# Optimization experiments

Measured on AMD Instinct MI355X. Metric: run time of the kernel, lower is better.

## Reference

```python
import jax, jax.numpy as jnp
import numpy as np

B, NV, NF, AOD, SD = 16384, 32, 64, 64, 512  # batch, num_variable, num_factor, adj_output_dim, state_dim
H = AOD * AOD // 2  # 2048, hyper_w1 hidden/out


def setup_inputs() -> dict:
    key = jax.random.key(0)
    ks = jax.random.split(key, 16)
    s = 0.02
    p = lambda k, shp: (s * jax.random.normal(k, shp, dtype=jnp.float32))
    return {
        "agent_emb": jax.random.normal(ks[0], (B, NV, AOD), dtype=jnp.float32),
        "states": jax.random.normal(ks[1], (B, SD), dtype=jnp.float32),
        # hyper_w1: Linear(SD,H) -> ReLU -> Linear(H,H)
        "w1a_W": p(ks[2], (SD, H)), "w1a_b": jnp.zeros((H,), jnp.float32),
        "w1b_W": p(ks[3], (H, H)), "w1b_b": jnp.zeros((H,), jnp.float32),
        # hyper_b1: Linear(SD, NV*AOD//2)
        "b1_W": p(ks[4], (SD, NV * AOD // 2)), "b1_b": jnp.zeros((NV * AOD // 2,), jnp.float32),
        # hyper_w2: Linear(SD, AOD//2*NF*2) -> ReLU -> Linear(.., AOD//2*NF)
        "w2a_W": p(ks[5], (SD, AOD // 2 * NF * 2)), "w2a_b": jnp.zeros((AOD // 2 * NF * 2,), jnp.float32),
        "w2b_W": p(ks[6], (AOD // 2 * NF * 2, AOD // 2 * NF)), "w2b_b": jnp.zeros((AOD // 2 * NF,), jnp.float32),
        # hyper_b2: Linear(SD, NV*AOD//2) -> ReLU -> Linear(.., NV*NF)
        "b2a_W": p(ks[7], (SD, NV * AOD // 2)), "b2a_b": jnp.zeros((NV * AOD // 2,), jnp.float32),
        "b2b_W": p(ks[8], (NV * AOD // 2, NV * NF)), "b2b_b": jnp.zeros((NV * NF,), jnp.float32),
    }


def reference(agent_emb, states, w1a_W, w1a_b, w1b_W, w1b_b, b1_W, b1_b,
              w2a_W, w2a_b, w2b_W, w2b_b, b2a_W, b2a_b, b2b_W, b2b_b):
    # hypernets
    w1 = (jax.nn.relu(states @ w1a_W + w1a_b) @ w1b_W + w1b_b).reshape(B, AOD, AOD // 2)
    b1 = (states @ b1_W + b1_b).reshape(B, NV, AOD // 2)
    w2 = (jax.nn.relu(states @ w2a_W + w2a_b) @ w2b_W + w2b_b).reshape(B, AOD // 2, NF)
    b2 = (jax.nn.relu(states @ b2a_W + b2a_b) @ b2b_W + b2b_b).reshape(B, NV, NF)
    # mixing: small batched matmuls + ELU
    hidden = jax.nn.elu(jnp.einsum('bva,bah->bvh', agent_emb, w1) + b1)  # [B,NV,AOD//2]
    out = jnp.einsum('bvh,bhf->bvf', hidden, w2) + b2                    # [B,NV,NF]
    # detached abs-max normalization over the variable dim, then sigmoid
    max_out = jax.lax.stop_gradient(jnp.max(jnp.abs(out), axis=1, keepdims=True)) + 1e-5
    norm = jnp.minimum(jnp.ones_like(max_out), 5.0 / max_out)
    return jax.nn.sigmoid(out * norm)
```

## Files before the change

### kernel.cpp

```cpp
#include <hip/hip_runtime.h>
#include <hip/hip_bf16.h>

#define B_    16384
#define NV_   32
#define NF_   64
#define AOD_  64
#define SD_   512
#define H_    2048
#define MC_   4096
#define NCHUNK_ 4

typedef __attribute__((ext_vector_type(8))) short short8_t;
typedef __attribute__((ext_vector_type(8))) unsigned short ushort8_t;
typedef __attribute__((ext_vector_type(4))) unsigned short ushort4_t;
typedef __attribute__((ext_vector_type(4))) float f32x4;

__device__ __forceinline__ float bf2f(unsigned short u) {
  union { unsigned int i; float f; } c; c.i = ((unsigned int)u) << 16; return c.f;
}
__device__ __forceinline__ unsigned short f2bf(float f) {
  union { float f; unsigned int i; } c; c.f = f;
  unsigned int x = c.i;
  return (unsigned short)((x + 0x7FFFu + ((x >> 16) & 1u)) >> 16);
}

__device__ __forceinline__ void gload16(const unsigned short* g, unsigned short* l) {
  __builtin_amdgcn_global_load_lds(
      (const __attribute__((address_space(1))) unsigned int*)g,
      (__attribute__((address_space(3))) unsigned int*)l, 16, 0, 0);
}


__global__ __launch_bounds__(256) void transpose_split(
    const float* __restrict__ src, unsigned short* __restrict__ dhi,
    unsigned short* __restrict__ dlo, int K, int N) {
  __shared__ float tile[32][33];
  const int nb = blockIdx.x * 32, kb = blockIdx.y * 32;
  const int tx = threadIdx.x & 31, ty = threadIdx.x >> 5;
#pragma unroll
  for (int r = 0; r < 32; r += 8)
    tile[ty + r][tx] = src[(size_t)(kb + ty + r) * N + nb + tx];
  __syncthreads();
#pragma unroll
  for (int r = 0; r < 32; r += 8) {
    const float x = tile[tx][ty + r];
    const unsigned short h = f2bf(x);
    const size_t o = (size_t)(nb + ty + r) * K + kb + tx;
    dhi[o] = h;
    dlo[o] = f2bf(x - bf2f(h));
  }
}

__global__ __launch_bounds__(256) void transpose_single(
    const float* __restrict__ src, unsigned short* __restrict__ dst, int K, int N) {
  __shared__ float tile[32][33];
  const int nb = blockIdx.x * 32, kb = blockIdx.y * 32;
  const int tx = threadIdx.x & 31, ty = threadIdx.x >> 5;
#pragma unroll
  for (int r = 0; r < 32; r += 8)
    tile[ty + r][tx] = src[(size_t)(kb + ty + r) * N + nb + tx];
  __syncthreads();
#pragma unroll
  for (int r = 0; r < 32; r += 8)
    dst[(size_t)(nb + ty + r) * K + kb + tx] = f2bf(tile[tx][ty + r]);
}

__global__ __launch_bounds__(256) void cvt_split(
    const float* __restrict__ in, unsigned short* __restrict__ hi,
    unsigned short* __restrict__ lo) {
  const int i = (blockIdx.x * 256 + threadIdx.x) * 4;
  const float4 v = *(const float4*)(in + i);
  ushort4_t oh, ol;
  oh.x = f2bf(v.x); ol.x = f2bf(v.x - bf2f(oh.x));
  oh.y = f2bf(v.y); ol.y = f2bf(v.y - bf2f(oh.y));
  oh.z = f2bf(v.z); ol.z = f2bf(v.z - bf2f(oh.z));
  oh.w = f2bf(v.w); ol.w = f2bf(v.w - bf2f(oh.w));
  *(ushort4_t*)(hi + i) = oh;
  *(ushort4_t*)(lo + i) = ol;
}

template <int ASPLIT, int BSPLIT, int OMODE>
__global__ __launch_bounds__(256) void gemm_k(
    const unsigned short* __restrict__ Ah, const unsigned short* __restrict__ Al, int lda,
    const unsigned short* __restrict__ Bh, const unsigned short* __restrict__ Bl,
    const float* __restrict__ bias,
    void* __restrict__ outH, void* __restrict__ outL, int N, int K) {
  __shared__ unsigned short lAh[128 * 32];
  __shared__ unsigned short lBh[128 * 32];
  __shared__ unsigned short lAl[ASPLIT ? 128 * 32 : 64];
  __shared__ unsigned short lBl[BSPLIT ? 128 * 32 : 64];

  const int t = threadIdx.x;
  const int w = t >> 6, l = t & 63;
  const int wm = w >> 1, wn = w & 1;
  const int lhi = l >> 4, llo = l & 15;
  const int k8 = lhi * 8;
  const int m0 = blockIdx.y * 128, n0 = blockIdx.x * 128;

  const int r1 = t >> 2, kc = (t & 3) * 8;
  const size_t aoff1 = (size_t)(m0 + r1) * lda + kc;
  const size_t aoff2 = (size_t)(m0 + r1 + 64) * lda + kc;
  const size_t boff1 = (size_t)(n0 + r1) * (size_t)K + kc;
  const size_t boff2 = (size_t)(n0 + r1 + 64) * (size_t)K + kc;
  unsigned short* const d1 = (unsigned short*)0 + w * 512;
  const int wo1 = w * 512, wo2 = 2048 + w * 512;
  (void)d1;

  f32x4 acc[4][4];
#pragma unroll
  for (int i = 0; i < 4; ++i)
#pragma unroll
    for (int j = 0; j < 4; ++j) acc[i][j] = (f32x4){0.f, 0.f, 0.f, 0.f};

  for (int kt = 0; kt < K; kt += 32) {
    gload16(Ah + aoff1 + kt, lAh + wo1);
    gload16(Ah + aoff2 + kt, lAh + wo2);
    if constexpr (ASPLIT) {
      gload16(Al + aoff1 + kt, lAl + wo1);
      gload16(Al + aoff2 + kt, lAl + wo2);
    }
    gload16(Bh + boff1 + kt, lBh + wo1);
    gload16(Bh + boff2 + kt, lBh + wo2);
    if constexpr (BSPLIT) {
      gload16(Bl + boff1 + kt, lBl + wo1);
      gload16(Bl + boff2 + kt, lBl + wo2);
    }
    __syncthreads();

    short8_t ah[4], bh[4];
#pragma unroll
    for (int i = 0; i < 4; ++i)
      ah[i] = *(const short8_t*)&lAh[(wm * 64 + i * 16 + llo) * 32 + k8];
#pragma unroll
    for (int j = 0; j < 4; ++j)
      bh[j] = *(const short8_t*)&lBh[(wn * 64 + j * 16 + llo) * 32 + k8];

    if constexpr (ASPLIT && BSPLIT) {
      short8_t al[4], bl[4];
#pragma unroll
      for (int i = 0; i < 4; ++i)
        al[i] = *(const short8_t*)&lAl[(wm * 64 + i * 16 + llo) * 32 + k8];
#pragma unroll
      for (int j = 0; j < 4; ++j)
        bl[j] = *(const short8_t*)&lBl[(wn * 64 + j * 16 + llo) * 32 + k8];
#pragma unroll
      for (int i = 0; i < 4; ++i)
#pragma unroll
        for (int j = 0; j < 4; ++j) {
          acc[i][j] = __builtin_amdgcn_mfma_f32_16x16x32_bf16(ah[i], bh[j], acc[i][j], 0, 0, 0);
          acc[i][j] = __builtin_amdgcn_mfma_f32_16x16x32_bf16(ah[i], bl[j], acc[i][j], 0, 0, 0);
          acc[i][j] = __builtin_amdgcn_mfma_f32_16x16x32_bf16(al[i], bh[j], acc[i][j], 0, 0, 0);
        }
    } else {
#pragma unroll
      for (int i = 0; i < 4; ++i)
#pragma unroll
        for (int j = 0; j < 4; ++j)
          acc[i][j] = __builtin_amdgcn_mfma_f32_16x16x32_bf16(ah[i], bh[j], acc[i][j], 0, 0, 0);
    }
    __syncthreads();
  }

#pragma unroll
  for (int j = 0; j < 4; ++j) {
    const int col = n0 + wn * 64 + j * 16 + llo;
    const float bv = bias[col];
#pragma unroll
    for (int i = 0; i < 4; ++i) {
      const int row = m0 + wm * 64 + i * 16 + lhi * 4;
#pragma unroll
      for (int r = 0; r < 4; ++r) {
        float v = acc[i][j][r] + bv;
        if constexpr (OMODE == 1 || OMODE == 2) v = fmaxf(v, 0.f);
        const size_t o = (size_t)(row + r) * N + col;
        if constexpr (OMODE == 3) {
          ((float*)outH)[o] = v;
        } else if constexpr (OMODE == 2) {
          const unsigned short h = f2bf(v);
          ((unsigned short*)outH)[o] = h;
          ((unsigned short*)outL)[o] = f2bf(v - bf2f(h));
        } else {
          ((unsigned short*)outH)[o] = f2bf(v);
        }
      }
    }
  }
}

__global__ __launch_bounds__(256) void mixing_kernel(
    const float* __restrict__ emb,
    const float* __restrict__ w1buf,
    const unsigned short* __restrict__ b1buf,
    const float* __restrict__ w2buf,
    const unsigned short* __restrict__ b2buf,
    float* __restrict__ out) {
  __shared__ float s_emb[2048];
  __shared__ float s_w1[2048];
  __shared__ float s_b1[1024];
  __shared__ float s_w2[2048];
  __shared__ float s_b2[2048];
  __shared__ float s_hid[1024];
  __shared__ float s_out[2048];
  __shared__ float s_norm[64];

  const int b = blockIdx.x, t = threadIdx.x;

  {
    const float4* src = (const float4*)(emb + (size_t)b * 2048);
    ((float4*)s_emb)[t] = src[t];
    ((float4*)s_emb)[t + 256] = src[t + 256];
  }
  {
    const float4* src = (const float4*)(w1buf + (size_t)b * 2048);
    ((float4*)s_w1)[t] = src[t];
    ((float4*)s_w1)[t + 256] = src[t + 256];
  }
  {
    const float4* src = (const float4*)(w2buf + (size_t)b * 2048);
    ((float4*)s_w2)[t] = src[t];
    ((float4*)s_w2)[t + 256] = src[t + 256];
  }
  if (t < 128) {
    ushort8_t u = *(const ushort8_t*)(b1buf + (size_t)b * 1024 + t * 8);
#pragma unroll
    for (int e = 0; e < 8; ++e) s_b1[t * 8 + e] = bf2f(u[e]);
  }
  {
    ushort8_t u = *(const ushort8_t*)(b2buf + (size_t)b * 2048 + t * 8);
#pragma unroll
    for (int e = 0; e < 8; ++e) s_b2[t * 8 + e] = bf2f(u[e]);
  }
  __syncthreads();

#pragma unroll
  for (int p = 0; p < 4; ++p) {
    const int idx = t + p * 256;
    const int v = idx >> 5, h = idx & 31;
    float acc = s_b1[idx];
#pragma unroll 8
    for (int a = 0; a < 64; ++a) acc += s_emb[v * 64 + a] * s_w1[a * 32 + h];
    s_hid[idx] = acc > 0.f ? acc : expm1f(acc);
  }
  __syncthreads();

#pragma unroll
  for (int p = 0; p < 8; ++p) {
    const int idx = t + p * 256;
    const int v = idx >> 6, f = idx & 63;
    float acc = s_b2[idx];
#pragma unroll 8
    for (int h = 0; h < 32; ++h) acc += s_hid[v * 32 + h] * s_w2[h * 64 + f];
    s_out[idx] = acc;
  }
  __syncthreads();

  if (t < 64) {
    float m = 0.f;
#pragma unroll
    for (int v = 0; v < 32; ++v) m = fmaxf(m, fabsf(s_out[v * 64 + t]));
    m += 1e-5f;
    s_norm[t] = fminf(1.0f, 5.0f / m);
  }
  __syncthreads();

#pragma unroll
  for (int p = 0; p < 8; ++p) {
    const int idx = t + p * 256;
    const float x = s_out[idx] * s_norm[idx & 63];
    out[(size_t)b * 2048 + idx] = 1.f / (1.f + expf(-x));
  }
}


extern "C" void kernel_launch(void* const* d_in, const int* in_sizes, int n_in,
                              void* d_out, int out_size, void* d_ws, size_t ws_size,
                              hipStream_t stream) {
  const float* agent_emb = (const float*)d_in[0];
  const float* states    = (const float*)d_in[1];
  const float* w1a_W = (const float*)d_in[2];  const float* w1a_b = (const float*)d_in[3];
  const float* w1b_W = (const float*)d_in[4];  const float* w1b_b = (const float*)d_in[5];
  const float* b1_W  = (const float*)d_in[6];  const float* b1_b  = (const float*)d_in[7];
  const float* w2a_W = (const float*)d_in[8];  const float* w2a_b = (const float*)d_in[9];
  const float* w2b_W = (const float*)d_in[10]; const float* w2b_b = (const float*)d_in[11];
  const float* b2a_W = (const float*)d_in[12]; const float* b2a_b = (const float*)d_in[13];
  const float* b2b_W = (const float*)d_in[14]; const float* b2b_b = (const float*)d_in[15];
  float* out = (float*)d_out;

  char* ws = (char*)d_ws;
  size_t off = 0;
  auto alloc = [&](size_t bytes) -> char* {
    char* p = ws + off;
    off = (off + bytes + 255) & ~(size_t)255;
    return p;
  };
  typedef unsigned short us;
  us* sth = (us*)alloc((size_t)B_ * SD_ * 2);
  us* stl = (us*)alloc((size_t)B_ * SD_ * 2);
  us* w1aTh = (us*)alloc((size_t)2048 * 512 * 2); us* w1aTl = (us*)alloc((size_t)2048 * 512 * 2);
  us* b1Th  = (us*)alloc((size_t)1024 * 512 * 2); us* b1Tl  = (us*)alloc((size_t)1024 * 512 * 2);
  us* w2aTh = (us*)alloc((size_t)4096 * 512 * 2); us* w2aTl = (us*)alloc((size_t)4096 * 512 * 2);
  us* b2aTh = (us*)alloc((size_t)1024 * 512 * 2); us* b2aTl = (us*)alloc((size_t)1024 * 512 * 2);
  us* w1bTh = (us*)alloc((size_t)2048 * 2048 * 2); us* w1bTl = (us*)alloc((size_t)2048 * 2048 * 2);
  us* w2bTh = (us*)alloc((size_t)2048 * 4096 * 2); us* w2bTl = (us*)alloc((size_t)2048 * 4096 * 2);
  us* b2bT  = (us*)alloc((size_t)2048 * 1024 * 2);
  us* t1h = (us*)alloc((size_t)MC_ * 2048 * 2); us* t1l = (us*)alloc((size_t)MC_ * 2048 * 2);
  us* t2h = (us*)alloc((size_t)MC_ * 4096 * 2); us* t2l = (us*)alloc((size_t)MC_ * 4096 * 2);
  us* b1buf = (us*)alloc((size_t)MC_ * 1024 * 2);
  us* t3buf = (us*)alloc((size_t)MC_ * 1024 * 2);
  float* w1buf = (float*)alloc((size_t)MC_ * 2048 * 4);
  float* w2buf = (float*)alloc((size_t)MC_ * 2048 * 4);
  us* b2buf = (us*)alloc((size_t)MC_ * 2048 * 2);
  if (off > ws_size) return;

  cvt_split<<<(B_ * SD_) / (4 * 256), 256, 0, stream>>>(states, sth, stl);
  transpose_split<<<dim3(2048 / 32, 512 / 32), 256, 0, stream>>>(w1a_W, w1aTh, w1aTl, 512, 2048);
  transpose_split<<<dim3(1024 / 32, 512 / 32), 256, 0, stream>>>(b1_W,  b1Th,  b1Tl,  512, 1024);
  transpose_split<<<dim3(4096 / 32, 512 / 32), 256, 0, stream>>>(w2a_W, w2aTh, w2aTl, 512, 4096);
  transpose_split<<<dim3(1024 / 32, 512 / 32), 256, 0, stream>>>(b2a_W, b2aTh, b2aTl, 512, 1024);
  transpose_split<<<dim3(2048 / 32, 2048 / 32), 256, 0, stream>>>(w1b_W, w1bTh, w1bTl, 2048, 2048);
  transpose_split<<<dim3(2048 / 32, 4096 / 32), 256, 0, stream>>>(w2b_W, w2bTh, w2bTl, 4096, 2048);
  transpose_single<<<dim3(2048 / 32, 1024 / 32), 256, 0, stream>>>(b2b_W, b2bT, 1024, 2048);

  for (int c = 0; c < NCHUNK_; ++c) {
    const size_t R = (size_t)c * MC_;
    const us* Ah = sth + R * SD_;
    const us* Al = stl + R * SD_;
    gemm_k<1, 1, 2><<<dim3(16, MC_ / 128), 256, 0, stream>>>(
        Ah, Al, SD_, w1aTh, w1aTl, w1a_b, t1h, t1l, 2048, SD_);
    gemm_k<1, 1, 0><<<dim3(8, MC_ / 128), 256, 0, stream>>>(
        Ah, Al, SD_, b1Th, b1Tl, b1_b, b1buf, nullptr, 1024, SD_);
    gemm_k<1, 1, 2><<<dim3(32, MC_ / 128), 256, 0, stream>>>(
        Ah, Al, SD_, w2aTh, w2aTl, w2a_b, t2h, t2l, 4096, SD_);
    gemm_k<1, 1, 1><<<dim3(8, MC_ / 128), 256, 0, stream>>>(
        Ah, Al, SD_, b2aTh, b2aTl, b2a_b, t3buf, nullptr, 1024, SD_);
    gemm_k<1, 1, 3><<<dim3(16, MC_ / 128), 256, 0, stream>>>(
        t1h, t1l, 2048, w1bTh, w1bTl, w1b_b, w1buf, nullptr, 2048, 2048);
    gemm_k<1, 1, 3><<<dim3(16, MC_ / 128), 256, 0, stream>>>(
        t2h, t2l, 4096, w2bTh, w2bTl, w2b_b, w2buf, nullptr, 2048, 4096);
    gemm_k<0, 0, 0><<<dim3(16, MC_ / 128), 256, 0, stream>>>(
        t3buf, nullptr, 1024, b2bT, nullptr, b2b_b, b2buf, nullptr, 2048, 1024);
    mixing_kernel<<<MC_, 256, 0, stream>>>(
        agent_emb + R * 2048, w1buf, b1buf, w2buf, b2buf, out + R * 2048);
  }
}
```

Before: 2.511 ms.

## Rewrite GEMMs as 256x256 multi-stage pipelined kernels and vectorize mixing

Replaces the 128x128 bf16x3 GEMM with a 256x256-tile, 512-thread kernel. It streams the hi/lo split terms as extra K segments through a 4-deep LDS ring buffer loaded with global_load_lds, using swizzled LDS offsets, XCD-aware block remapping and raised wave priority around the MFMA block. The chunk size doubles to 8192 rows, so there are fewer launches. The mixing kernel gets padded LDS arrays and register-blocked, float4-vectorized inner loops with rotated indices to avoid bank conflicts. Costs: 128KB of dynamic LDS per block and higher register pressure, which may limit occupancy. Workspace needs also grow with the larger chunk.

```diff
diff --git a/kernel.cpp b/kernel.cpp
--- a/kernel.cpp
+++ b/kernel.cpp
@@ -7,24 +7,25 @@
 #define AOD_  64
 #define SD_   512
 #define H_    2048
-#define MC_   4096
-#define NCHUNK_ 4
-
+#define MC_   8192
+#define NCHUNK_ 2
+
+typedef unsigned short us;
 typedef __attribute__((ext_vector_type(8))) short short8_t;
 typedef __attribute__((ext_vector_type(8))) unsigned short ushort8_t;
 typedef __attribute__((ext_vector_type(4))) unsigned short ushort4_t;
 typedef __attribute__((ext_vector_type(4))) float f32x4;
 
-__device__ __forceinline__ float bf2f(unsigned short u) {
+__device__ __forceinline__ float bf2f(us u) {
   union { unsigned int i; float f; } c; c.i = ((unsigned int)u) << 16; return c.f;
 }
-__device__ __forceinline__ unsigned short f2bf(float f) {
+__device__ __forceinline__ us f2bf(float f) {
   union { float f; unsigned int i; } c; c.f = f;
   unsigned int x = c.i;
-  return (unsigned short)((x + 0x7FFFu + ((x >> 16) & 1u)) >> 16);
-}
-
-__device__ __forceinline__ void gload16(const unsigned short* g, unsigned short* l) {
+  return (us)((x + 0x7FFFu + ((x >> 16) & 1u)) >> 16);
+}
+
+__device__ __forceinline__ void gload16(const us* g, us* l) {
   __builtin_amdgcn_global_load_lds(
       (const __attribute__((address_space(1))) unsigned int*)g,
       (__attribute__((address_space(3))) unsigned int*)l, 16, 0, 0);
@@ -32,8 +33,8 @@
 
 
 __global__ __launch_bounds__(256) void transpose_split(
-    const float* __restrict__ src, unsigned short* __restrict__ dhi,
-    unsigned short* __restrict__ dlo, int K, int N) {
+    const float* __restrict__ src, us* __restrict__ dhi,
+    us* __restrict__ dlo, int K, int N) {
   __shared__ float tile[32][33];
   const int nb = blockIdx.x * 32, kb = blockIdx.y * 32;
   const int tx = threadIdx.x & 31, ty = threadIdx.x >> 5;
@@ -44,7 +45,7 @@
 #pragma unroll
   for (int r = 0; r < 32; r += 8) {
     const float x = tile[tx][ty + r];
-    const unsigned short h = f2bf(x);
+    const us h = f2bf(x);
     const size_t o = (size_t)(nb + ty + r) * K + kb + tx;
     dhi[o] = h;
     dlo[o] = f2bf(x - bf2f(h));
@@ -52,7 +53,7 @@
 }
 
 __global__ __launch_bounds__(256) void transpose_single(
-    const float* __restrict__ src, unsigned short* __restrict__ dst, int K, int N) {
+    const float* __restrict__ src, us* __restrict__ dst, int K, int N) {
   __shared__ float tile[32][33];
   const int nb = blockIdx.x * 32, kb = blockIdx.y * 32;
   const int tx = threadIdx.x & 31, ty = threadIdx.x >> 5;
@@ -66,8 +67,7 @@
 }
 
 __global__ __launch_bounds__(256) void cvt_split(
-    const float* __restrict__ in, unsigned short* __restrict__ hi,
-    unsigned short* __restrict__ lo) {
+    const float* __restrict__ in, us* __restrict__ hi, us* __restrict__ lo) {
   const int i = (blockIdx.x * 256 + threadIdx.x) * 4;
   const float4 v = *(const float4*)(in + i);
   ushort4_t oh, ol;
@@ -79,86 +79,97 @@
   *(ushort4_t*)(lo + i) = ol;
 }
 
-template <int ASPLIT, int BSPLIT, int OMODE>
-__global__ __launch_bounds__(256) void gemm_k(
-    const unsigned short* __restrict__ Ah, const unsigned short* __restrict__ Al, int lda,
-    const unsigned short* __restrict__ Bh, const unsigned short* __restrict__ Bl,
+template <int SPLIT, int OMODE>
+__global__ __launch_bounds__(512, 2) void gemm8(
+    const us* __restrict__ Ah, const us* __restrict__ Al, int lda,
+    const us* __restrict__ Bh, const us* __restrict__ Bl, int ldb,
     const float* __restrict__ bias,
-    void* __restrict__ outH, void* __restrict__ outL, int N, int K) {
-  __shared__ unsigned short lAh[128 * 32];
-  __shared__ unsigned short lBh[128 * 32];
-  __shared__ unsigned short lAl[ASPLIT ? 128 * 32 : 64];
-  __shared__ unsigned short lBl[BSPLIT ? 128 * 32 : 64];
+    void* __restrict__ outH, void* __restrict__ outL, int N, int KK, int gx) {
+  extern __shared__ __align__(16) char smem[];
 
   const int t = threadIdx.x;
   const int w = t >> 6, l = t & 63;
-  const int wm = w >> 1, wn = w & 1;
-  const int lhi = l >> 4, llo = l & 15;
-  const int k8 = lhi * 8;
-  const int m0 = blockIdx.y * 128, n0 = blockIdx.x * 128;
-
-  const int r1 = t >> 2, kc = (t & 3) * 8;
-  const size_t aoff1 = (size_t)(m0 + r1) * lda + kc;
-  const size_t aoff2 = (size_t)(m0 + r1 + 64) * lda + kc;
-  const size_t boff1 = (size_t)(n0 + r1) * (size_t)K + kc;
-  const size_t boff2 = (size_t)(n0 + r1 + 64) * (size_t)K + kc;
-  unsigned short* const d1 = (unsigned short*)0 + w * 512;
-  const int wo1 = w * 512, wo2 = 2048 + w * 512;
-  (void)d1;
-
-  f32x4 acc[4][4];
-#pragma unroll
-  for (int i = 0; i < 4; ++i)
+  const int wm = w >> 2, wn = w & 3;
+  const int llo = l & 15, lhi = l >> 4;
+
+  const int nwg = gridDim.x;
+  const int q = nwg >> 3, r = nwg & 7;
+  const int xcd = blockIdx.x & 7, idx = blockIdx.x >> 3;
+  const int wg = (xcd < r ? xcd * (q + 1) : r * (q + 1) + (xcd - r) * q) + idx;
+  const int bx = wg % gx, by = wg / gx;
+  const int m0 = by * 256, n0 = bx * 256;
+
+  const int s1 = t + 512;
+  const int rowA0 = t >> 2, rowA1 = s1 >> 2;
+  const int ch0 = (t & 3) ^ (rowA0 & 3), ch1 = (s1 & 3) ^ (rowA1 & 3);
+  const size_t aoff0 = (size_t)(m0 + rowA0) * lda + ch0 * 8;
+  const size_t aoff1 = (size_t)(m0 + rowA1) * lda + ch1 * 8;
+  const size_t boff0 = (size_t)(n0 + rowA0) * ldb + ch0 * 8;
+  const size_t boff1 = (size_t)(n0 + rowA1) * ldb + ch1 * 8;
+  const int wbase = w * 1024;
+
+  int offA[8], offB[4];
+#pragma unroll
+  for (int i = 0; i < 8; ++i) {
+    const int rr = wm * 128 + i * 16 + llo;
+    offA[i] = (rr * 64 + lhi * 16) ^ ((llo & 3) << 4);
+  }
+#pragma unroll
+  for (int j = 0; j < 4; ++j) {
+    const int rr = wn * 64 + j * 16 + llo;
+    offB[j] = ((rr * 64 + lhi * 16) ^ ((llo & 3) << 4)) + 16384;
+  }
+
+  const int NT = (SPLIT ? 3 : 1) * (KK / 32);
+
+  auto stage = [&](int tile) {
+    int ko;
+    const us *As, *Bs;
+    if constexpr (SPLIT) {
+      const int kt = tile * 32;
+      const int seg = (kt >= KK) + (kt >= 2 * KK);
+      ko = kt - seg * KK;
+      As = (seg == 1) ? Al : Ah;
+      Bs = (seg == 2) ? Bl : Bh;
+    } else {
+      ko = tile * 32; As = Ah; Bs = Bh;
+    }
+    char* base = smem + (tile & 3) * 32768;
+    gload16(As + aoff0 + ko, (us*)(base + wbase));
+    gload16(As + aoff1 + ko, (us*)(base + 8192 + wbase));
+    gload16(Bs + boff0 + ko, (us*)(base + 16384 + wbase));
+    gload16(Bs + boff1 + ko, (us*)(base + 16384 + 8192 + wbase));
+  };
+
+  f32x4 acc[8][4];
+#pragma unroll
+  for (int i = 0; i < 8; ++i)
 #pragma unroll
     for (int j = 0; j < 4; ++j) acc[i][j] = (f32x4){0.f, 0.f, 0.f, 0.f};
 
-  for (int kt = 0; kt < K; kt += 32) {
-    gload16(Ah + aoff1 + kt, lAh + wo1);
-    gload16(Ah + aoff2 + kt, lAh + wo2);
-    if constexpr (ASPLIT) {
-      gload16(Al + aoff1 + kt, lAl + wo1);
-      gload16(Al + aoff2 + kt, lAl + wo2);
-    }
-    gload16(Bh + boff1 + kt, lBh + wo1);
-    gload16(Bh + boff2 + kt, lBh + wo2);
-    if constexpr (BSPLIT) {
-      gload16(Bl + boff1 + kt, lBl + wo1);
-      gload16(Bl + boff2 + kt, lBl + wo2);
-    }
-    __syncthreads();
-
-    short8_t ah[4], bh[4];
-#pragma unroll
-    for (int i = 0; i < 4; ++i)
-      ah[i] = *(const short8_t*)&lAh[(wm * 64 + i * 16 + llo) * 32 + k8];
-#pragma unroll
-    for (int j = 0; j < 4; ++j)
-      bh[j] = *(const short8_t*)&lBh[(wn * 64 + j * 16 + llo) * 32 + k8];
-
-    if constexpr (ASPLIT && BSPLIT) {
-      short8_t al[4], bl[4];
-#pragma unroll
-      for (int i = 0; i < 4; ++i)
-        al[i] = *(const short8_t*)&lAl[(wm * 64 + i * 16 + llo) * 32 + k8];
+  stage(0); stage(1); stage(2);
+  asm volatile("s_waitcnt vmcnt(8)" ::: "memory");
+  __builtin_amdgcn_s_barrier();
+  __builtin_amdgcn_sched_barrier(0);
+
+  for (int tt = 0; tt < NT; ++tt) {
+    if (tt + 3 < NT) stage(tt + 3);
+    const char* base = smem + (tt & 3) * 32768;
+    short8_t af[8], bf[4];
+#pragma unroll
+    for (int i = 0; i < 8; ++i) af[i] = *(const short8_t*)(base + offA[i]);
+#pragma unroll
+    for (int j = 0; j < 4; ++j) bf[j] = *(const short8_t*)(base + offB[j]);
+    __builtin_amdgcn_s_setprio(1);
+#pragma unroll
+    for (int i = 0; i < 8; ++i)
 #pragma unroll
       for (int j = 0; j < 4; ++j)
-        bl[j] = *(const short8_t*)&lBl[(wn * 64 + j * 16 + llo) * 32 + k8];
-#pragma unroll
-      for (int i = 0; i < 4; ++i)
-#pragma unroll
-        for (int j = 0; j < 4; ++j) {
-          acc[i][j] = __builtin_amdgcn_mfma_f32_16x16x32_bf16(ah[i], bh[j], acc[i][j], 0, 0, 0);
-          acc[i][j] = __builtin_amdgcn_mfma_f32_16x16x32_bf16(ah[i], bl[j], acc[i][j], 0, 0, 0);
-          acc[i][j] = __builtin_amdgcn_mfma_f32_16x16x32_bf16(al[i], bh[j], acc[i][j], 0, 0, 0);
-        }
-    } else {
-#pragma unroll
-      for (int i = 0; i < 4; ++i)
-#pragma unroll
-        for (int j = 0; j < 4; ++j)
-          acc[i][j] = __builtin_amdgcn_mfma_f32_16x16x32_bf16(ah[i], bh[j], acc[i][j], 0, 0, 0);
-    }
-    __syncthreads();
+        acc[i][j] = __builtin_amdgcn_mfma_f32_16x16x32_bf16(af[i], bf[j], acc[i][j], 0, 0, 0);
+    __builtin_amdgcn_s_setprio(0);
+    asm volatile("s_waitcnt vmcnt(8)" ::: "memory");
+    __builtin_amdgcn_s_barrier();
+    __builtin_amdgcn_sched_barrier(0);
   }
 
 #pragma unroll
@@ -166,21 +177,21 @@
     const int col = n0 + wn * 64 + j * 16 + llo;
     const float bv = bias[col];
 #pragma unroll
-    for (int i = 0; i < 4; ++i) {
-      const int row = m0 + wm * 64 + i * 16 + lhi * 4;
-#pragma unroll
-      for (int r = 0; r < 4; ++r) {
-        float v = acc[i][j][r] + bv;
+    for (int i = 0; i < 8; ++i) {
+      const int row = m0 + wm * 128 + i * 16 + lhi * 4;
+#pragma unroll
+      for (int rr = 0; rr < 4; ++rr) {
+        float v = acc[i][j][rr] + bv;
         if constexpr (OMODE == 1 || OMODE == 2) v = fmaxf(v, 0.f);
-        const size_t o = (size_t)(row + r) * N + col;
+        const size_t o = (size_t)(row + rr) * N + col;
         if constexpr (OMODE == 3) {
           ((float*)outH)[o] = v;
         } else if constexpr (OMODE == 2) {
-          const unsigned short h = f2bf(v);
-          ((unsigned short*)outH)[o] = h;
-          ((unsigned short*)outL)[o] = f2bf(v - bf2f(h));
+          const us h = f2bf(v);
+          ((us*)outH)[o] = h;
+          ((us*)outL)[o] = f2bf(v - bf2f(h));
         } else {
-          ((unsigned short*)outH)[o] = f2bf(v);
+          ((us*)outH)[o] = f2bf(v);
         }
       }
     }
@@ -190,16 +201,16 @@
 __global__ __launch_bounds__(256) void mixing_kernel(
     const float* __restrict__ emb,
     const float* __restrict__ w1buf,
-    const unsigned short* __restrict__ b1buf,
+    const us* __restrict__ b1buf,
     const float* __restrict__ w2buf,
-    const unsigned short* __restrict__ b2buf,
+    const us* __restrict__ b2buf,
     float* __restrict__ out) {
-  __shared__ float s_emb[2048];
+  __shared__ float s_emb[32 * 65];
   __shared__ float s_w1[2048];
   __shared__ float s_b1[1024];
   __shared__ float s_w2[2048];
   __shared__ float s_b2[2048];
-  __shared__ float s_hid[1024];
+  __shared__ float s_hid[32 * 33];
   __shared__ float s_out[2048];
   __shared__ float s_norm[64];
 
@@ -207,8 +218,13 @@
 
   {
     const float4* src = (const float4*)(emb + (size_t)b * 2048);
-    ((float4*)s_emb)[t] = src[t];
-    ((float4*)s_emb)[t + 256] = src[t + 256];
+#pragma unroll
+    for (int p = 0; p < 2; ++p) {
+      const int i4 = t + p * 256;
+      const float4 v = src[i4];
+      const int e = i4 * 4;
+      *(float4*)&s_emb[(e >> 6) * 65 + (e & 63)] = v;
+    }
   }
   {
     const float4* src = (const float4*)(w1buf + (size_t)b * 2048);
@@ -232,25 +248,43 @@
   }
   __syncthreads();
 
-#pragma unroll
-  for (int p = 0; p < 4; ++p) {
-    const int idx = t + p * 256;
-    const int v = idx >> 5, h = idx & 31;
-    float acc = s_b1[idx];
+  {
+    const int v = t >> 3, hq = t & 7;
+    float a0 = s_b1[v * 32 + hq * 4 + 0];
+    float a1 = s_b1[v * 32 + hq * 4 + 1];
+    float a2 = s_b1[v * 32 + hq * 4 + 2];
+    float a3 = s_b1[v * 32 + hq * 4 + 3];
 #pragma unroll 8
-    for (int a = 0; a < 64; ++a) acc += s_emb[v * 64 + a] * s_w1[a * 32 + h];
-    s_hid[idx] = acc > 0.f ? acc : expm1f(acc);
-  }
-  __syncthreads();
-
-#pragma unroll
-  for (int p = 0; p < 8; ++p) {
-    const int idx = t + p * 256;
-    const int v = idx >> 6, f = idx & 63;
-    float acc = s_b2[idx];
+    for (int aa = 0; aa < 64; ++aa) {
+      const int ai = (aa + hq * 8) & 63;
+      const float e = s_emb[v * 65 + ai];
+      const float4 wv = *(const float4*)&s_w1[ai * 32 + hq * 4];
+      a0 += e * wv.x; a1 += e * wv.y; a2 += e * wv.z; a3 += e * wv.w;
+    }
+    s_hid[v * 33 + hq * 4 + 0] = a0 > 0.f ? a0 : expm1f(a0);
+    s_hid[v * 33 + hq * 4 + 1] = a1 > 0.f ? a1 : expm1f(a1);
+    s_hid[v * 33 + hq * 4 + 2] = a2 > 0.f ? a2 : expm1f(a2);
+    s_hid[v * 33 + hq * 4 + 3] = a3 > 0.f ? a3 : expm1f(a3);
+  }
+  __syncthreads();
+
+  {
+    const int v = t >> 3, fo = t & 7;
+    float c[8];
+#pragma unroll
+    for (int k = 0; k < 8; ++k) c[k] = s_b2[v * 64 + fo * 8 + k];
 #pragma unroll 8
-    for (int h = 0; h < 32; ++h) acc += s_hid[v * 32 + h] * s_w2[h * 64 + f];
-    s_out[idx] = acc;
+    for (int hh = 0; hh < 32; ++hh) {
+      const int hi2 = (hh + fo * 4) & 31;
+      const float hv = s_hid[v * 33 + hi2];
+      const float4 w0 = *(const float4*)&s_w2[hi2 * 64 + fo * 8];
+      const float4 w1v = *(const float4*)&s_w2[hi2 * 64 + fo * 8 + 4];
+      c[0] += hv * w0.x; c[1] += hv * w0.y; c[2] += hv * w0.z; c[3] += hv * w0.w;
+      c[4] += hv * w1v.x; c[5] += hv * w1v.y; c[6] += hv * w1v.z; c[7] += hv * w1v.w;
+    }
+    float4 o0 = {c[0], c[1], c[2], c[3]}, o1 = {c[4], c[5], c[6], c[7]};
+    *(float4*)&s_out[v * 64 + fo * 8] = o0;
+    *(float4*)&s_out[v * 64 + fo * 8 + 4] = o1;
   }
   __syncthreads();
 
@@ -286,6 +320,12 @@
   const float* b2b_W = (const float*)d_in[14]; const float* b2b_b = (const float*)d_in[15];
   float* out = (float*)d_out;
 
+  hipFuncSetAttribute((const void*)(gemm8<1, 0>), hipFuncAttributeMaxDynamicSharedMemorySize, 131072);
+  hipFuncSetAttribute((const void*)(gemm8<1, 1>), hipFuncAttributeMaxDynamicSharedMemorySize, 131072);
+  hipFuncSetAttribute((const void*)(gemm8<1, 2>), hipFuncAttributeMaxDynamicSharedMemorySize, 131072);
+  hipFuncSetAttribute((const void*)(gemm8<1, 3>), hipFuncAttributeMaxDynamicSharedMemorySize, 131072);
+  hipFuncSetAttribute((const void*)(gemm8<0, 0>), hipFuncAttributeMaxDynamicSharedMemorySize, 131072);
+
   char* ws = (char*)d_ws;
   size_t off = 0;
   auto alloc = [&](size_t bytes) -> char* {
@@ -293,7 +333,6 @@
     off = (off + bytes + 255) & ~(size_t)255;
     return p;
   };
-  typedef unsigned short us;
   us* sth = (us*)alloc((size_t)B_ * SD_ * 2);
   us* stl = (us*)alloc((size_t)B_ * SD_ * 2);
   us* w1aTh = (us*)alloc((size_t)2048 * 512 * 2); us* w1aTl = (us*)alloc((size_t)2048 * 512 * 2);
@@ -325,20 +364,20 @@
     const size_t R = (size_t)c * MC_;
     const us* Ah = sth + R * SD_;
     const us* Al = stl + R * SD_;
-    gemm_k<1, 1, 2><<<dim3(16, MC_ / 128), 256, 0, stream>>>(
-        Ah, Al, SD_, w1aTh, w1aTl, w1a_b, t1h, t1l, 2048, SD_);
-    gemm_k<1, 1, 0><<<dim3(8, MC_ / 128), 256, 0, stream>>>(
-        Ah, Al, SD_, b1Th, b1Tl, b1_b, b1buf, nullptr, 1024, SD_);
-    gemm_k<1, 1, 2><<<dim3(32, MC_ / 128), 256, 0, stream>>>(
-        Ah, Al, SD_, w2aTh, w2aTl, w2a_b, t2h, t2l, 4096, SD_);
-    gemm_k<1, 1, 1><<<dim3(8, MC_ / 128), 256, 0, stream>>>(
-        Ah, Al, SD_, b2aTh, b2aTl, b2a_b, t3buf, nullptr, 1024, SD_);
-    gemm_k<1, 1, 3><<<dim3(16, MC_ / 128), 256, 0, stream>>>(
-        t1h, t1l, 2048, w1bTh, w1bTl, w1b_b, w1buf, nullptr, 2048, 2048);
-    gemm_k<1, 1, 3><<<dim3(16, MC_ / 128), 256, 0, stream>>>(
-        t2h, t2l, 4096, w2bTh, w2bTl, w2b_b, w2buf, nullptr, 2048, 4096);
-    gemm_k<0, 0, 0><<<dim3(16, MC_ / 128), 256, 0, stream>>>(
-        t3buf, nullptr, 1024, b2bT, nullptr, b2b_b, b2buf, nullptr, 2048, 1024);
+    gemm8<1, 2><<<(2048 / 256) * (MC_ / 256), 512, 131072, stream>>>(
+        Ah, Al, SD_, w1aTh, w1aTl, SD_, w1a_b, t1h, t1l, 2048, SD_, 2048 / 256);
+    gemm8<1, 0><<<(1024 / 256) * (MC_ / 256), 512, 131072, stream>>>(
+        Ah, Al, SD_, b1Th, b1Tl, SD_, b1_b, b1buf, nullptr, 1024, SD_, 1024 / 256);
+    gemm8<1, 2><<<(4096 / 256) * (MC_ / 256), 512, 131072, stream>>>(
+        Ah, Al, SD_, w2aTh, w2aTl, SD_, w2a_b, t2h, t2l, 4096, SD_, 4096 / 256);
+    gemm8<1, 1><<<(1024 / 256) * (MC_ / 256), 512, 131072, stream>>>(
+        Ah, Al, SD_, b2aTh, b2aTl, SD_, b2a_b, t3buf, nullptr, 1024, SD_, 1024 / 256);
+    gemm8<1, 3><<<(2048 / 256) * (MC_ / 256), 512, 131072, stream>>>(
+        t1h, t1l, 2048, w1bTh, w1bTl, 2048, w1b_b, w1buf, nullptr, 2048, 2048, 2048 / 256);
+    gemm8<1, 3><<<(2048 / 256) * (MC_ / 256), 512, 131072, stream>>>(
+        t2h, t2l, 4096, w2bTh, w2bTl, 4096, w2b_b, w2buf, nullptr, 2048, 4096, 2048 / 256);
+    gemm8<0, 0><<<(2048 / 256) * (MC_ / 256), 512, 131072, stream>>>(
+        t3buf, nullptr, 1024, b2bT, nullptr, 1024, b2b_b, b2buf, nullptr, 2048, 1024, 2048 / 256);
     mixing_kernel<<<MC_, 256, 0, stream>>>(
         agent_emb + R * 2048, w1buf, b1buf, w2buf, b2buf, out + R * 2048);
   }
```

After: 2.334 ms. 7.0% less time.
